# Performance work log

Hardware: AMD Instinct MI355X
Metric: run time of the kernel (lower is better)

The kernel has to match this reference:

```python
import jax, jax.numpy as jnp
import numpy as np

ALPHA = 3.0
EPS = 1e-6
LOSS_WEIGHT = 1.0
N = 1_000_000


def _cross(a, b):
    return a[..., 0] * b[..., 1] - a[..., 1] * b[..., 0]


def _corners(b):
    # b: (n,5) -> (n,4,2) corners in CCW-ish order
    x, y, w, h, a = (b[:, i] for i in range(5))
    c, s = jnp.cos(a), jnp.sin(a)
    dx = jnp.stack([-w, w, w, -w], -1) * 0.5  # (n,4)
    dy = jnp.stack([-h, -h, h, h], -1) * 0.5
    X = x[:, None] + dx * c[:, None] - dy * s[:, None]
    Y = y[:, None] + dx * s[:, None] + dy * c[:, None]
    return jnp.stack([X, Y], -1)


def _inside(pts, box):
    # pts: (n,4,2) world coords; box: (n,5). Test via box-local frame.
    x, y, w, h, a = (box[:, i] for i in range(5))
    c, s = jnp.cos(a), jnp.sin(a)
    rel = pts - jnp.stack([x, y], -1)[:, None]
    lx = rel[..., 0] * c[:, None] + rel[..., 1] * s[:, None]
    ly = -rel[..., 0] * s[:, None] + rel[..., 1] * c[:, None]
    m = 1e-5  # numeric margin
    return (jnp.abs(lx) <= w[:, None] * 0.5 + m) & (jnp.abs(ly) <= h[:, None] * 0.5 + m)


def _rot_inter_area(b1, b2):
    c1, c2 = _corners(b1), _corners(b2)            # (n,4,2)
    r = jnp.roll(c1, -1, axis=1) - c1               # edge vectors box1
    s = jnp.roll(c2, -1, axis=1) - c2               # edge vectors box2
    p = c1[:, :, None]                              # (n,4,1,2)
    q = c2[:, None]                                 # (n,1,4,2)
    rr = r[:, :, None]
    ss = s[:, None]
    den = _cross(rr, ss)                            # (n,4,4)
    den_safe = jnp.where(jnp.abs(den) < 1e-12, 1.0, den)
    qp = q - p
    t = _cross(qp, ss) / den_safe
    u = _cross(qp, rr) / den_safe
    ok = (jnp.abs(den) > 1e-12) & (t >= 0.0) & (t <= 1.0) & (u >= 0.0) & (u <= 1.0)
    ipts = p + t[..., None] * rr                    # (n,4,4,2) edge-edge intersections

    n = b1.shape[0]
    pts = jnp.concatenate([ipts.reshape(n, 16, 2), c1, c2], axis=1)          # (n,24,2)
    mask = jnp.concatenate([ok.reshape(n, 16), _inside(c1, b2), _inside(c2, b1)], axis=1)
    maskf = mask.astype(pts.dtype)
    cnt = maskf.sum(1)                              # (n,)
    center = (pts * maskf[..., None]).sum(1) / jnp.maximum(cnt, 1.0)[:, None]

    ang = jnp.arctan2(pts[..., 1] - center[:, None, 1], pts[..., 0] - center[:, None, 0])
    ang = jnp.where(mask, ang, 1e9)                 # invalid points sort last
    order = jnp.argsort(ang, axis=1)
    pts_s = jnp.take_along_axis(pts, order[..., None], axis=1)
    mask_s = jnp.take_along_axis(mask, order, axis=1)
    first = pts_s[:, 0:1]
    pts_s = jnp.where(mask_s[..., None], pts_s, first)  # collapse invalid -> zero shoelace terms
    nxt = jnp.roll(pts_s, -1, axis=1)
    area = 0.5 * jnp.abs(_cross(pts_s, nxt).sum(1))
    return jnp.where(cnt >= 3.0, area, 0.0)


def setup_inputs() -> dict:
    key = jax.random.key(0)
    k1, k2, k3, k4, k5, k6 = jax.random.split(key, 6)
    xy = jax.random.uniform(k1, (N, 2), jnp.float32, 0.0, 512.0)
    wh = jax.random.uniform(k2, (N, 2), jnp.float32, 4.0, 64.0)
    ang = jax.random.uniform(k3, (N, 1), jnp.float32, -np.pi / 2, np.pi / 2)
    pred = jnp.concatenate([xy, wh, ang], axis=1)
    # target: perturbed pred so IoUs are non-trivial
    txy = xy + jax.random.normal(k4, (N, 2), jnp.float32) * 4.0
    twh = wh * jax.random.uniform(k5, (N, 2), jnp.float32, 0.8, 1.25)
    tang = ang + jax.random.normal(k6, (N, 1), jnp.float32) * 0.2
    target = jnp.concatenate([txy, twh, tang], axis=1)
    return {"pred": pred, "target": target}


def reference(pred, target):
    inter = _rot_inter_area(pred, target)
    a1 = pred[:, 2] * pred[:, 3]
    a2 = target[:, 2] * target[:, 3]
    ious = inter / (a1 + a2 - inter)
    ious = jnp.maximum(ious, EPS)                   # clamp(min=eps)
    loss = 1.0 - ious ** ALPHA                      # linear=True branch
    return LOSS_WEIGHT * loss.mean()                # reduction='mean'
```

## Files before the change

kernel.cpp:

```cpp
#include <hip/hip_runtime.h>
#include <math.h>

#define EPS_IOU 1e-6f
#define BLOCK 256
#define BPT 4
#define EPB (BLOCK * BPT)

__device__ __forceinline__ float clip_len(float p0x, float p0y, float dx, float dy,
                                          float rcx, float rcy, float ux, float uy,
                                          float hw, float hh) {
  const float rx = p0x - rcx, ry = p0y - rcy;
  const float bu = rx * ux + ry * uy;
  const float bv = -rx * uy + ry * ux;
  const float au = dx * ux + dy * uy;
  const float av = -dx * uy + dy * ux;
  const float iu = __builtin_amdgcn_rcpf(au);
  const float iv = __builtin_amdgcn_rcpf(av);
  const float t0 = (-hw - bu) * iu;
  const float t1 = (hw - bu) * iu;
  const float t2 = (-hh - bv) * iv;
  const float t3 = (hh - bv) * iv;
  const float lo = fmaxf(fmaxf(fminf(t0, t1), fminf(t2, t3)), 0.0f);
  const float hi = fminf(fminf(fmaxf(t0, t1), fmaxf(t2, t3)), 1.0f);
  return fmaxf(hi - lo, 0.0f);
}

__device__ __forceinline__ float pair_loss(const float* b1, const float* b2) {
  const float x1 = b1[0], y1 = b1[1], w1 = b1[2], h1 = b1[3], t1 = b1[4];
  const float x2 = b2[0], y2 = b2[1], w2 = b2[2], h2 = b2[3], t2 = b2[4];

  float s1, c1, s2, c2;
  __sincosf(t1, &s1, &c1);
  __sincosf(t2, &s2, &c2);

  const float ox = 0.5f * (x1 + x2), oy = 0.5f * (y1 + y2);
  const float a1x = x1 - ox, a1y = y1 - oy;
  const float a2x = x2 - ox, a2y = y2 - oy;

  const float hw1 = 0.5f * w1, hh1 = 0.5f * h1;
  const float hw2 = 0.5f * w2, hh2 = 0.5f * h2;

  float Ax[4], Ay[4], Bx[4], By[4];
  {
    const float dxs1[4] = {-hw1, hw1, hw1, -hw1};
    const float dys1[4] = {-hh1, -hh1, hh1, hh1};
    const float dxs2[4] = {-hw2, hw2, hw2, -hw2};
    const float dys2[4] = {-hh2, -hh2, hh2, hh2};
#pragma unroll
    for (int k = 0; k < 4; ++k) {
      Ax[k] = a1x + dxs1[k] * c1 - dys1[k] * s1;
      Ay[k] = a1y + dxs1[k] * s1 + dys1[k] * c1;
      Bx[k] = a2x + dxs2[k] * c2 - dys2[k] * s2;
      By[k] = a2y + dxs2[k] * s2 + dys2[k] * c2;
    }
  }

  float acc = 0.0f;
#pragma unroll
  for (int k = 0; k < 4; ++k) {
    const int kn = (k + 1) & 3;
    {
      const float dx = Ax[kn] - Ax[k], dy = Ay[kn] - Ay[k];
      const float len = clip_len(Ax[k], Ay[k], dx, dy, a2x, a2y, c2, s2, hw2, hh2);
      acc += (Ax[k] * dy - Ay[k] * dx) * len;
    }
    {
      const float dx = Bx[kn] - Bx[k], dy = By[kn] - By[k];
      const float len = clip_len(Bx[k], By[k], dx, dy, a1x, a1y, c1, s1, hw1, hh1);
      acc += (Bx[k] * dy - By[k] * dx) * len;
    }
  }
  const float inter = fmaxf(0.5f * acc, 0.0f);

  const float uni = w1 * h1 + w2 * h2 - inter;
  float iou = inter * __builtin_amdgcn_rcpf(uni);
  iou = fmaxf(iou, EPS_IOU);
  return 1.0f - iou * iou * iou;
}

__global__ __launch_bounds__(256) void rot_iou_loss_kernel(
    const float* __restrict__ pred, const float* __restrict__ target,
    float* __restrict__ block_sums, int n) {
  const int tid = threadIdx.x;
  const long g0 = ((long)blockIdx.x * BLOCK + tid) * BPT;

  float loss = 0.0f;
  if (g0 + BPT - 1 < n) {
    float fp[20], ft[20];
    const float4* p4 = (const float4*)(pred + g0 * 5);
    const float4* t4 = (const float4*)(target + g0 * 5);
#pragma unroll
    for (int q = 0; q < 5; ++q) {
      ((float4*)fp)[q] = p4[q];
      ((float4*)ft)[q] = t4[q];
    }
#pragma unroll
    for (int j = 0; j < BPT; ++j) loss += pair_loss(&fp[j * 5], &ft[j * 5]);
  } else {
#pragma unroll
    for (int j = 0; j < BPT; ++j) {
      const long gi = g0 + j;
      if (gi < n) {
        float bp[5], bt[5];
#pragma unroll
        for (int k = 0; k < 5; ++k) {
          bp[k] = pred[gi * 5 + k];
          bt[k] = target[gi * 5 + k];
        }
        loss += pair_loss(bp, bt);
      }
    }
  }

#pragma unroll
  for (int off = 32; off > 0; off >>= 1) loss += __shfl_down(loss, off, 64);

  __shared__ float wsum[4];
  const int lane = tid & 63;
  const int wid = tid >> 6;
  if (lane == 0) wsum[wid] = loss;
  __syncthreads();
  if (tid == 0) {
    block_sums[blockIdx.x] = wsum[0] + wsum[1] + wsum[2] + wsum[3];
  }
}

__global__ __launch_bounds__(256) void final_reduce_kernel(
    const float* __restrict__ block_sums, float* __restrict__ out, int nb,
    float inv_n) {
  const int tid = threadIdx.x;
  float s = 0.0f;
  for (int i = tid; i < nb; i += 256) s += block_sums[i];
#pragma unroll
  for (int off = 32; off > 0; off >>= 1) s += __shfl_down(s, off, 64);

  __shared__ float wsum[4];
  const int lane = tid & 63;
  const int wid = tid >> 6;
  if (lane == 0) wsum[wid] = s;
  __syncthreads();
  if (tid == 0) out[0] = (wsum[0] + wsum[1] + wsum[2] + wsum[3]) * inv_n;
}

extern "C" void kernel_launch(void* const* d_in, const int* in_sizes, int n_in,
                              void* d_out, int out_size, void* d_ws, size_t ws_size,
                              hipStream_t stream) {
  const float* pred = (const float*)d_in[0];
  const float* target = (const float*)d_in[1];
  float* out = (float*)d_out;
  float* bsums = (float*)d_ws;
  const int n = in_sizes[0] / 5;

  const int grid = (n + EPB - 1) / EPB;
  rot_iou_loss_kernel<<<grid, BLOCK, 0, stream>>>(pred, target, bsums, n);
  final_reduce_kernel<<<1, BLOCK, 0, stream>>>(bsums, out, grid,
                                               1.0f / (float)n);
}
```

Before: 90.00 us.

## Compute clipped-edge intersection in relative frames and reduce via atomics

Rewrites the intersection-area math to work in each box's local axis-aligned frame, using the relative angle. Edge clipping becomes an axis-aligned slab test with reciprocals shared across opposite edges, and the shoelace sum is expressed in closed form, which cuts per-pair arithmetic. The second-stage reduction kernel is replaced by a per-block atomicAdd into the output plus a tiny zeroing kernel. The float atomics make the summation order nondeterministic.

```diff
diff --git a/kernel.cpp b/kernel.cpp
--- a/kernel.cpp
+++ b/kernel.cpp
@@ -6,81 +6,83 @@
 #define BPT 4
 #define EPB (BLOCK * BPT)
 
-__device__ __forceinline__ float clip_len(float p0x, float p0y, float dx, float dy,
-                                          float rcx, float rcy, float ux, float uy,
-                                          float hw, float hh) {
-  const float rx = p0x - rcx, ry = p0y - rcy;
-  const float bu = rx * ux + ry * uy;
-  const float bv = -rx * uy + ry * ux;
-  const float au = dx * ux + dy * uy;
-  const float av = -dx * uy + dy * ux;
-  const float iu = __builtin_amdgcn_rcpf(au);
-  const float iv = __builtin_amdgcn_rcpf(av);
-  const float t0 = (-hw - bu) * iu;
-  const float t1 = (hw - bu) * iu;
-  const float t2 = (-hh - bv) * iv;
-  const float t3 = (hh - bv) * iv;
+__global__ void zero_out_kernel(float* out) { out[0] = 0.0f; }
+
+__device__ __forceinline__ float clip_aa(float px, float py, float idx, float idy,
+                                         float hw, float hh) {
+  const float t0 = (-hw - px) * idx;
+  const float t1 = ( hw - px) * idx;
+  const float t2 = (-hh - py) * idy;
+  const float t3 = ( hh - py) * idy;
   const float lo = fmaxf(fmaxf(fminf(t0, t1), fminf(t2, t3)), 0.0f);
   const float hi = fminf(fminf(fmaxf(t0, t1), fmaxf(t2, t3)), 1.0f);
   return fmaxf(hi - lo, 0.0f);
 }
 
 __device__ __forceinline__ float pair_loss(const float* b1, const float* b2) {
-  const float x1 = b1[0], y1 = b1[1], w1 = b1[2], h1 = b1[3], t1 = b1[4];
-  const float x2 = b2[0], y2 = b2[1], w2 = b2[2], h2 = b2[3], t2 = b2[4];
+  const float x1 = b1[0], y1 = b1[1], hw1 = 0.5f * b1[2], hh1 = 0.5f * b1[3];
+  const float x2 = b2[0], y2 = b2[1], hw2 = 0.5f * b2[2], hh2 = 0.5f * b2[3];
 
-  float s1, c1, s2, c2;
-  __sincosf(t1, &s1, &c1);
-  __sincosf(t2, &s2, &c2);
+  float s2v, c2v, sf, cf;
+  __sincosf(b2[4], &s2v, &c2v);
+  __sincosf(b1[4] - b2[4], &sf, &cf);
 
-  const float ox = 0.5f * (x1 + x2), oy = 0.5f * (y1 + y2);
-  const float a1x = x1 - ox, a1y = y1 - oy;
-  const float a2x = x2 - ox, a2y = y2 - oy;
+  const float dx = x1 - x2, dy = y1 - y2;
+  const float qx = c2v * dx + s2v * dy;
+  const float qy = -s2v * dx + c2v * dy;
+  const float qpx = -(cf * qx + sf * qy);
+  const float qpy = sf * qx - cf * qy;
 
-  const float hw1 = 0.5f * w1, hh1 = 0.5f * h1;
-  const float hw2 = 0.5f * w2, hh2 = 0.5f * h2;
+  const float e1x = hw1 * cf, e1y = hw1 * sf;
+  const float e2x = -hh1 * sf, e2y = hh1 * cf;
+  const float f1x = hw2 * cf, f1y = -hw2 * sf;
+  const float f2x = hh2 * sf, f2y = hh2 * cf;
 
-  float Ax[4], Ay[4], Bx[4], By[4];
-  {
-    const float dxs1[4] = {-hw1, hw1, hw1, -hw1};
-    const float dys1[4] = {-hh1, -hh1, hh1, hh1};
-    const float dxs2[4] = {-hw2, hw2, hw2, -hw2};
-    const float dys2[4] = {-hh2, -hh2, hh2, hh2};
-#pragma unroll
-    for (int k = 0; k < 4; ++k) {
-      Ax[k] = a1x + dxs1[k] * c1 - dys1[k] * s1;
-      Ay[k] = a1y + dxs1[k] * s1 + dys1[k] * c1;
-      Bx[k] = a2x + dxs2[k] * c2 - dys2[k] * s2;
-      By[k] = a2y + dxs2[k] * s2 + dys2[k] * c2;
-    }
-  }
+  const float P0x = qx - e1x - e2x, P0y = qy - e1y - e2y;
+  const float P1x = qx + e1x - e2x, P1y = qy + e1y - e2y;
+  const float P2x = qx + e1x + e2x, P2y = qy + e1y + e2y;
+  const float P3x = qx - e1x + e2x, P3y = qy - e1y + e2y;
+  const float Q0x = qpx - f1x - f2x, Q0y = qpy - f1y - f2y;
+  const float Q1x = qpx + f1x - f2x, Q1y = qpy + f1y - f2y;
+  const float Q2x = qpx + f1x + f2x, Q2y = qpy + f1y + f2y;
+  const float Q3x = qpx - f1x + f2x, Q3y = qpy - f1y + f2y;
 
-  float acc = 0.0f;
-#pragma unroll
-  for (int k = 0; k < 4; ++k) {
-    const int kn = (k + 1) & 3;
-    {
-      const float dx = Ax[kn] - Ax[k], dy = Ay[kn] - Ay[k];
-      const float len = clip_len(Ax[k], Ay[k], dx, dy, a2x, a2y, c2, s2, hw2, hh2);
-      acc += (Ax[k] * dy - Ay[k] * dx) * len;
-    }
-    {
-      const float dx = Bx[kn] - Bx[k], dy = By[kn] - By[k];
-      const float len = clip_len(Bx[k], By[k], dx, dy, a1x, a1y, c1, s1, hw1, hh1);
-      acc += (Bx[k] * dy - By[k] * dx) * len;
-    }
-  }
-  const float inter = fmaxf(0.5f * acc, 0.0f);
+  const float i1x = __builtin_amdgcn_rcpf(2.0f * e1x);
+  const float i1y = __builtin_amdgcn_rcpf(2.0f * e1y);
+  const float i2x = __builtin_amdgcn_rcpf(2.0f * e2x);
+  const float i2y = __builtin_amdgcn_rcpf(2.0f * e2y);
+  const float j1x = __builtin_amdgcn_rcpf(2.0f * f1x);
+  const float j1y = __builtin_amdgcn_rcpf(2.0f * f1y);
+  const float j2x = __builtin_amdgcn_rcpf(2.0f * f2x);
+  const float j2y = __builtin_amdgcn_rcpf(2.0f * f2y);
 
-  const float uni = w1 * h1 + w2 * h2 - inter;
-  float iou = inter * __builtin_amdgcn_rcpf(uni);
+  const float L0 = clip_aa(P0x, P0y, i1x, i1y, hw2, hh2);
+  const float L1 = clip_aa(P1x, P1y, i2x, i2y, hw2, hh2);
+  const float L2 = clip_aa(P2x, P2y, -i1x, -i1y, hw2, hh2);
+  const float L3 = clip_aa(P3x, P3y, -i2x, -i2y, hw2, hh2);
+  const float M0 = clip_aa(Q0x, Q0y, j1x, j1y, hw1, hh1);
+  const float M1 = clip_aa(Q1x, Q1y, j2x, j2y, hw1, hh1);
+  const float M2 = clip_aa(Q2x, Q2y, -j1x, -j1y, hw1, hh1);
+  const float M3 = clip_aa(Q3x, Q3y, -j2x, -j2y, hw1, hh1);
+
+  const float alpha = 2.0f * (qx * e1y - qy * e1x);
+  const float beta = 2.0f * (qx * e2y - qy * e2x);
+  const float gA = 2.0f * hw1 * hh1;
+  const float gB = 2.0f * hw2 * hh2;
+  const float S = gA * (L0 + L1 + L2 + L3) + alpha * (L0 - L2) +
+                  beta * (L1 - L3) + gB * (M0 + M1 + M2 + M3);
+  const float inter = fmaxf(0.5f * S, 0.0f);
+
+  const float a1 = 4.0f * hw1 * hh1;
+  const float a2 = 4.0f * hw2 * hh2;
+  float iou = inter * __builtin_amdgcn_rcpf(a1 + a2 - inter);
   iou = fmaxf(iou, EPS_IOU);
   return 1.0f - iou * iou * iou;
 }
 
 __global__ __launch_bounds__(256) void rot_iou_loss_kernel(
     const float* __restrict__ pred, const float* __restrict__ target,
-    float* __restrict__ block_sums, int n) {
+    float* __restrict__ out, int n, float inv_n) {
   const int tid = threadIdx.x;
   const long g0 = ((long)blockIdx.x * BLOCK + tid) * BPT;
 
@@ -121,25 +123,8 @@
   if (lane == 0) wsum[wid] = loss;
   __syncthreads();
   if (tid == 0) {
-    block_sums[blockIdx.x] = wsum[0] + wsum[1] + wsum[2] + wsum[3];
+    atomicAdd(out, (wsum[0] + wsum[1] + wsum[2] + wsum[3]) * inv_n);
   }
-}
-
-__global__ __launch_bounds__(256) void final_reduce_kernel(
-    const float* __restrict__ block_sums, float* __restrict__ out, int nb,
-    float inv_n) {
-  const int tid = threadIdx.x;
-  float s = 0.0f;
-  for (int i = tid; i < nb; i += 256) s += block_sums[i];
-#pragma unroll
-  for (int off = 32; off > 0; off >>= 1) s += __shfl_down(s, off, 64);
-
-  __shared__ float wsum[4];
-  const int lane = tid & 63;
-  const int wid = tid >> 6;
-  if (lane == 0) wsum[wid] = s;
-  __syncthreads();
-  if (tid == 0) out[0] = (wsum[0] + wsum[1] + wsum[2] + wsum[3]) * inv_n;
 }
 
 extern "C" void kernel_launch(void* const* d_in, const int* in_sizes, int n_in,
@@ -148,11 +133,10 @@
   const float* pred = (const float*)d_in[0];
   const float* target = (const float*)d_in[1];
   float* out = (float*)d_out;
-  float* bsums = (float*)d_ws;
   const int n = in_sizes[0] / 5;
 
+  zero_out_kernel<<<1, 1, 0, stream>>>(out);
   const int grid = (n + EPB - 1) / EPB;
-  rot_iou_loss_kernel<<<grid, BLOCK, 0, stream>>>(pred, target, bsums, n);
-  final_reduce_kernel<<<1, BLOCK, 0, stream>>>(bsums, out, grid,
-                                               1.0f / (float)n);
+  rot_iou_loss_kernel<<<grid, BLOCK, 0, stream>>>(pred, target, out, n,
+                                                  1.0f / (float)n);
 }
```

Result: no change. 90.33 us (+0.4%).
